# Kernel optimization log

Hardware: AMD Instinct MI355X
Metric: run time of the kernel (lower is better)

Reference implementation:

```python
import jax, jax.numpy as jnp
import numpy as np

N = 50000      # nodes
E = 800000     # edges (avg degree 16)
DIN = 128
HID = 128
OUT = 10       # classes
G = 64         # graphs in batch


def setup_inputs() -> dict:
    key = jax.random.key(0)
    ks = jax.random.split(key, 10)
    x = jax.random.normal(ks[0], (N, DIN), dtype=jnp.float32)
    edge_index = jax.random.randint(ks[1], (2, E), 0, N, dtype=jnp.int32)
    edge_weight = jax.random.uniform(ks[2], (E,), dtype=jnp.float32)
    batch = jnp.sort(jax.random.randint(ks[3], (N,), 0, G, dtype=jnp.int32))
    W1 = jax.random.normal(ks[4], (DIN, HID), dtype=jnp.float32) / np.sqrt(DIN)
    b1 = jnp.zeros((HID,), dtype=jnp.float32)
    W2 = jax.random.normal(ks[5], (HID, HID), dtype=jnp.float32) / np.sqrt(HID)
    b2 = jnp.zeros((HID,), dtype=jnp.float32)
    W3 = jax.random.normal(ks[6], (HID, OUT), dtype=jnp.float32) / np.sqrt(HID)
    b3 = jnp.zeros((OUT,), dtype=jnp.float32)
    return {"x": x, "edge_index": edge_index, "edge_weight": edge_weight,
            "batch": batch, "W1": W1, "b1": b1, "W2": W2, "b2": b2,
            "W3": W3, "b3": b3}


def _gcn_norm(edge_index, edge_weight, n_nodes):
    # PyG gcn_norm: add self-loops with weight 1, D^-1/2 (A+I) D^-1/2
    loop = jnp.arange(n_nodes, dtype=edge_index.dtype)
    src = jnp.concatenate([edge_index[0], loop])
    dst = jnp.concatenate([edge_index[1], loop])
    w = jnp.concatenate([edge_weight, jnp.ones((n_nodes,), edge_weight.dtype)])
    deg = jax.ops.segment_sum(w, dst, num_segments=n_nodes)
    dinv = jnp.where(deg > 0, jax.lax.rsqrt(deg), 0.0)
    norm = dinv[src] * w * dinv[dst]
    return src, dst, norm


def _gcn_conv(x, W, b, src, dst, norm, n_nodes):
    h = x @ W                                      # [N, F] dense transform
    msg = norm[:, None] * h[src]                   # gather + scale  [E+N, F]
    out = jax.ops.segment_sum(msg, dst, num_segments=n_nodes)  # scatter-add
    return out + b


def reference(x, edge_index, edge_weight, batch, W1, b1, W2, b2, W3, b3):
    src, dst, norm = _gcn_norm(edge_index, edge_weight, N)
    h = jax.nn.relu(_gcn_conv(x, W1, b1, src, dst, norm, N))
    h = jax.nn.relu(_gcn_conv(h, W2, b2, src, dst, norm, N))
    h = _gcn_conv(h, W3, b3, src, dst, norm, N)    # [N, OUT]
    # global_mean_pool over graph ids
    sums = jax.ops.segment_sum(h, batch, num_segments=G)          # [G, OUT]
    cnts = jax.ops.segment_sum(jnp.ones((N,), h.dtype), batch, num_segments=G)
    pooled = sums / jnp.maximum(cnts, 1.0)[:, None]
    return jax.nn.log_softmax(pooled, axis=1)
```

## Files before the change

### kernel.cpp

```cpp
#include <hip/hip_runtime.h>
#include <math.h>

#define NN 50000
#define EE 800000
#define GG 64
#define FD 128
#define OUTD 10
#define GB 782
#define BB 196
#define NBU 196
#define NBK 128
#define CH 6250
#define RCAP 8
#define TB 64

typedef __attribute__((ext_vector_type(8))) short s8v;
typedef __attribute__((ext_vector_type(4))) float f4v;

static __device__ inline unsigned short f2b(float f) {
    unsigned int u = __float_as_uint(f);
    return (unsigned short)((u + 0x7FFFu + ((u >> 16) & 1u)) >> 16);
}


__global__ __launch_bounds__(256) void k_histbounds(const float* __restrict__ W1,
        const float* __restrict__ W2, const float* __restrict__ W3,
        unsigned short* __restrict__ Wt1, unsigned short* __restrict__ Wt2,
        float* __restrict__ W3t, const int* __restrict__ dst, int* __restrict__ cnt2d,
        const int* __restrict__ batch, int* __restrict__ gstart) {
    int b = blockIdx.x;
    int tid = threadIdx.x;
    if (b < TB) {
        int i = b * 256 + tid;
        if (i < FD * FD) {
            int nn = i >> 7, k = i & 127;
            Wt1[i] = f2b(W1[k * FD + nn]);
            Wt2[i] = f2b(W2[k * FD + nn]);
        }
        if (i < FD * OUTD) {
            int col = i >> 7, row = i & 127;
            W3t[i] = W3[row * OUTD + col];
        }
    } else if (b < TB + NBK) {
        __shared__ unsigned hist[NBU];
        int blk = b - TB;
        if (tid < NBU) hist[tid] = 0;
        __syncthreads();
        int e0 = blk * CH;
        for (int e = e0 + tid; e < e0 + CH; e += 256)
            atomicAdd(&hist[(unsigned)dst[e] >> 8], 1u);
        __syncthreads();
        if (tid < NBU) cnt2d[tid * NBK + blk] = (int)hist[tid];
    } else {
        int i = (b - TB - NBK) * 256 + tid;
        if (i < NN) {
            int bb = batch[i];
            int bp = (i == 0) ? -1 : batch[i - 1];
            for (int g = bp + 1; g <= bb; ++g) gstart[g] = i;
            if (i == NN - 1)
                for (int g = bb + 1; g <= GG; ++g) gstart[g] = NN;
        }
    }
}


static __device__ inline void gemm_f32in_body(int bid, const float* __restrict__ A,
        const unsigned short* __restrict__ Wt, unsigned short* __restrict__ out, int n) {
    int tid = threadIdx.x;
    int wave = tid >> 6, lane = tid & 63;
    int quad = lane >> 4, c16 = lane & 15;
    int rowbase = bid * 64 + wave * 16;
    int rowA = rowbase + c16;
    if (rowA >= n) rowA = n - 1;
    f4v acc[8];
    #pragma unroll
    for (int t = 0; t < 8; ++t) acc[t] = (f4v){0.f, 0.f, 0.f, 0.f};
    #pragma unroll
    for (int k0 = 0; k0 < 128; k0 += 32) {
        const float* ap = A + (size_t)rowA * FD + k0 + quad * 8;
        float4 a0 = *(const float4*)ap;
        float4 a1 = *(const float4*)(ap + 4);
        s8v a;
        a[0] = (short)f2b(a0.x); a[1] = (short)f2b(a0.y);
        a[2] = (short)f2b(a0.z); a[3] = (short)f2b(a0.w);
        a[4] = (short)f2b(a1.x); a[5] = (short)f2b(a1.y);
        a[6] = (short)f2b(a1.z); a[7] = (short)f2b(a1.w);
        #pragma unroll
        for (int t = 0; t < 8; ++t) {
            s8v bb = *(const s8v*)(Wt + (size_t)(t * 16 + c16) * FD + k0 + quad * 8);
            acc[t] = __builtin_amdgcn_mfma_f32_16x16x32_bf16(a, bb, acc[t], 0, 0, 0);
        }
    }
    #pragma unroll
    for (int t = 0; t < 8; ++t) {
        #pragma unroll
        for (int r = 0; r < 4; ++r) {
            int row = rowbase + quad * 4 + r;
            if (row < n) out[(size_t)row * FD + t * 16 + c16] = f2b(acc[t][r]);
        }
    }
}

__global__ __launch_bounds__(256) void k_scatgemm(const int* __restrict__ src,
        const int* __restrict__ dst, const float* __restrict__ ew,
        const int* __restrict__ cnt2d, int* __restrict__ bbase_g, uint2* __restrict__ rec,
        const float* __restrict__ x, const unsigned short* __restrict__ Wt1,
        unsigned short* __restrict__ hA) {
    int b = blockIdx.x;
    int tid = threadIdx.x;
    if (b >= NBK) {
        gemm_f32in_body(b - NBK, x, Wt1, hA, NN);
        return;
    }
    __shared__ int colsum[NBU];
    __shared__ int ownoff[NBU];
    __shared__ unsigned cur[NBU];
    __shared__ int wtot_s[4];
    int blk = b;
    if (tid < NBU) {
        const int* c = cnt2d + tid * NBK;
        int own = 0, tot = 0;
        for (int k = 0; k < NBK; ++k) {
            int t = c[k];
            if (k < blk) own += t;
            tot += t;
        }
        ownoff[tid] = own;
        colsum[tid] = tot;
    }
    __syncthreads();
    {
        int lane = tid & 63, wv = tid >> 6;
        int v = (tid < NBU) ? colsum[tid] : 0;
        int s = v;
        #pragma unroll
        for (int off = 1; off < 64; off <<= 1) {
            int u = __shfl_up(s, off, 64);
            if (lane >= off) s += u;
        }
        if (lane == 63) wtot_s[wv] = s;
        __syncthreads();
        int pre = 0;
        for (int j = 0; j < wv; ++j) pre += wtot_s[j];
        int base = pre + s - v;
        if (tid < NBU) {
            cur[tid] = (unsigned)(base + ownoff[tid]);
            if (blk == 0) bbase_g[tid] = base;
        }
        if (blk == 0 && tid == NBU - 1) bbase_g[NBU] = base + v;
    }
    __syncthreads();
    int e0 = blk * CH;
    for (int e = e0 + tid; e < e0 + CH; e += 256) {
        int d = dst[e];
        unsigned bkt = (unsigned)d >> 8;
        unsigned pos = atomicAdd(&cur[bkt], 1u);
        rec[pos] = make_uint2(((unsigned)(d & 255) << 16) | (unsigned)src[e],
                              __float_as_uint(ew[e]));
    }
}


__global__ __launch_bounds__(1024) void k_rankfill(const uint2* __restrict__ rec,
        const int* __restrict__ bbase, int* __restrict__ rowptr, float* __restrict__ dinv_g,
        uint2* __restrict__ ent, unsigned short* __restrict__ rankb) {
    __shared__ unsigned cntS[256];
    __shared__ float wdegS[256];
    __shared__ int wtot_s[4];
    __shared__ int rowS[256];
    __shared__ float dinvS[256];
    int b = blockIdx.x;
    int tid = threadIdx.x;
    if (tid < 256) { cntS[tid] = 0; wdegS[tid] = 0.0f; }
    __syncthreads();
    int beg = bbase[b], end = bbase[b + 1];
    int s0 = beg + tid;
    uint2 rv[RCAP];
    unsigned rk[RCAP];
    #pragma unroll
    for (int k = 0; k < RCAP; ++k) {
        int s = s0 + k * 1024;
        if (s < end) {
            uint2 r = rec[s];
            unsigned dl = r.x >> 16;
            unsigned old = atomicAdd(&cntS[dl], 1u);
            atomicAdd(&wdegS[dl], __uint_as_float(r.y));
            rv[k] = r; rk[k] = old;
        }
    }
    for (int s = s0 + RCAP * 1024; s < end; s += 1024) {
        uint2 r = rec[s];
        unsigned dl = r.x >> 16;
        unsigned old = atomicAdd(&cntS[dl], 1u);
        atomicAdd(&wdegS[dl], __uint_as_float(r.y));
        rankb[s] = (unsigned short)old;
    }
    __syncthreads();
    {
        int lane = tid & 63, wv = tid >> 6;
        int v = (tid < 256) ? (int)cntS[tid] : 0;
        int s = v;
        #pragma unroll
        for (int off = 1; off < 64; off <<= 1) {
            int u = __shfl_up(s, off, 64);
            if (lane >= off) s += u;
        }
        if (tid < 256 && lane == 63) wtot_s[wv] = s;
        __syncthreads();
        if (tid < 256) {
            int pre = 0;
            for (int j = 0; j < wv; ++j) pre += wtot_s[j];
            int excl = pre + s - v;
            int node = b * 256 + tid;
            if (node < NN) {
                int r = beg + node + excl;
                rowS[tid] = r;
                rowptr[node] = r;
                float di = 1.0f / sqrtf(wdegS[tid] + 1.0f);
                dinvS[tid] = di;
                dinv_g[node] = di;
                ent[r + v] = make_uint2((unsigned)node, __float_as_uint(di));
            }
            if (node == NN - 1) rowptr[NN] = EE + NN;
        }
    }
    __syncthreads();
    #pragma unroll
    for (int k = 0; k < RCAP; ++k) {
        int s = s0 + k * 1024;
        if (s < end) {
            uint2 r = rv[k];
            unsigned dl = r.x >> 16;
            int pos = rowS[dl] + (int)rk[k];
            float val = __uint_as_float(r.y) * dinvS[dl];
            ent[pos] = make_uint2(r.x & 0xFFFFu, __float_as_uint(val));
        }
    }
    for (int s = s0 + RCAP * 1024; s < end; s += 1024) {
        uint2 r = rec[s];
        unsigned dl = r.x >> 16;
        int pos = rowS[dl] + (int)rankb[s];
        float val = __uint_as_float(r.y) * dinvS[dl];
        ent[pos] = make_uint2(r.x & 0xFFFFu, __float_as_uint(val));
    }
}


__global__ __launch_bounds__(256) void k_spmm_bf(const int* __restrict__ rowptr,
        const uint2* __restrict__ ent, const float* __restrict__ dinv,
        const unsigned short* __restrict__ tin, const float* __restrict__ bias,
        unsigned short* __restrict__ out, int n) {
    int w = (blockIdx.x * blockDim.x + threadIdx.x) >> 6;
    int lane = threadIdx.x & 63;
    if (w >= n) return;
    int c = lane & 15, g = lane >> 4;
    int beg = rowptr[w], end = rowptr[w + 1];
    float acc[8];
    #pragma unroll
    for (int j = 0; j < 8; ++j) acc[j] = 0.0f;
    int e0 = beg;
    for (; e0 + 16 <= end; e0 += 16) {
        uint2 en[4];
        float dv[4];
        uint4 t[4];
        #pragma unroll
        for (int u = 0; u < 4; ++u) en[u] = ent[e0 + 4 * u + g];
        #pragma unroll
        for (int u = 0; u < 4; ++u) dv[u] = dinv[en[u].x];
        #pragma unroll
        for (int u = 0; u < 4; ++u)
            t[u] = *(const uint4*)(tin + (size_t)en[u].x * FD + c * 8);
        #pragma unroll
        for (int u = 0; u < 4; ++u) {
            float v = __uint_as_float(en[u].y) * dv[u];
            acc[0] += v * __uint_as_float(t[u].x << 16);
            acc[1] += v * __uint_as_float(t[u].x & 0xFFFF0000u);
            acc[2] += v * __uint_as_float(t[u].y << 16);
            acc[3] += v * __uint_as_float(t[u].y & 0xFFFF0000u);
            acc[4] += v * __uint_as_float(t[u].z << 16);
            acc[5] += v * __uint_as_float(t[u].z & 0xFFFF0000u);
            acc[6] += v * __uint_as_float(t[u].w << 16);
            acc[7] += v * __uint_as_float(t[u].w & 0xFFFF0000u);
        }
    }
    for (; e0 < end; e0 += 4) {
        int e = e0 + g;
        uint2 en = (e < end) ? ent[e] : make_uint2(0u, 0u);
        float v = (e < end) ? __uint_as_float(en.y) * dinv[en.x] : 0.0f;
        uint4 t = *(const uint4*)(tin + (size_t)en.x * FD + c * 8);
        acc[0] += v * __uint_as_float(t.x << 16);
        acc[1] += v * __uint_as_float(t.x & 0xFFFF0000u);
        acc[2] += v * __uint_as_float(t.y << 16);
        acc[3] += v * __uint_as_float(t.y & 0xFFFF0000u);
        acc[4] += v * __uint_as_float(t.z << 16);
        acc[5] += v * __uint_as_float(t.z & 0xFFFF0000u);
        acc[6] += v * __uint_as_float(t.w << 16);
        acc[7] += v * __uint_as_float(t.w & 0xFFFF0000u);
    }
    #pragma unroll
    for (int j = 0; j < 8; ++j) {
        acc[j] += __shfl_xor(acc[j], 16, 64);
        acc[j] += __shfl_xor(acc[j], 32, 64);
    }
    if (g == 0) {
        float dself = dinv[w];
        uint4 r;
        float o[8];
        #pragma unroll
        for (int j = 0; j < 8; ++j)
            o[j] = fmaxf(acc[j] + bias[c * 8 + j], 0.0f) * dself;
        r.x = (unsigned)f2b(o[0]) | ((unsigned)f2b(o[1]) << 16);
        r.y = (unsigned)f2b(o[2]) | ((unsigned)f2b(o[3]) << 16);
        r.z = (unsigned)f2b(o[4]) | ((unsigned)f2b(o[5]) << 16);
        r.w = (unsigned)f2b(o[6]) | ((unsigned)f2b(o[7]) << 16);
        *(uint4*)(out + (size_t)w * FD + c * 8) = r;
    }
}


__global__ __launch_bounds__(256) void k_gemm_bf(const unsigned short* __restrict__ A,
        const unsigned short* __restrict__ Wt, unsigned short* __restrict__ out, int n) {
    int tid = threadIdx.x;
    int wave = tid >> 6, lane = tid & 63;
    int quad = lane >> 4, c16 = lane & 15;
    int rowbase = blockIdx.x * 64 + wave * 16;
    int rowA = rowbase + c16;
    if (rowA >= n) rowA = n - 1;
    f4v acc[8];
    #pragma unroll
    for (int t = 0; t < 8; ++t) acc[t] = (f4v){0.f, 0.f, 0.f, 0.f};
    #pragma unroll
    for (int k0 = 0; k0 < 128; k0 += 32) {
        s8v a = *(const s8v*)(A + (size_t)rowA * FD + k0 + quad * 8);
        #pragma unroll
        for (int t = 0; t < 8; ++t) {
            s8v b = *(const s8v*)(Wt + (size_t)(t * 16 + c16) * FD + k0 + quad * 8);
            acc[t] = __builtin_amdgcn_mfma_f32_16x16x32_bf16(a, b, acc[t], 0, 0, 0);
        }
    }
    #pragma unroll
    for (int t = 0; t < 8; ++t) {
        #pragma unroll
        for (int r = 0; r < 4; ++r) {
            int row = rowbase + quad * 4 + r;
            if (row < n) out[(size_t)row * FD + t * 16 + c16] = f2b(acc[t][r]);
        }
    }
}


__global__ __launch_bounds__(256) void k_spmm_w3(const int* __restrict__ rowptr,
        const uint2* __restrict__ ent, const float* __restrict__ dinv,
        const unsigned short* __restrict__ tin, const float* __restrict__ bias2,
        const float* __restrict__ W3t, float* __restrict__ outc, int n) {
    int tid = threadIdx.x;
    int w = (blockIdx.x * blockDim.x + tid) >> 6;
    int lane = tid & 63;
    if (w >= n) return;
    int c = lane & 15, g = lane >> 4;
    int beg = rowptr[w], end = rowptr[w + 1];
    float acc[8];
    #pragma unroll
    for (int j = 0; j < 8; ++j) acc[j] = 0.0f;
    int e0 = beg;
    for (; e0 + 16 <= end; e0 += 16) {
        uint2 en[4];
        uint4 t[4];
        #pragma unroll
        for (int u = 0; u < 4; ++u) en[u] = ent[e0 + 4 * u + g];
        #pragma unroll
        for (int u = 0; u < 4; ++u)
            t[u] = *(const uint4*)(tin + (size_t)en[u].x * FD + c * 8);
        #pragma unroll
        for (int u = 0; u < 4; ++u) {
            float v = __uint_as_float(en[u].y);
            acc[0] += v * __uint_as_float(t[u].x << 16);
            acc[1] += v * __uint_as_float(t[u].x & 0xFFFF0000u);
            acc[2] += v * __uint_as_float(t[u].y << 16);
            acc[3] += v * __uint_as_float(t[u].y & 0xFFFF0000u);
            acc[4] += v * __uint_as_float(t[u].z << 16);
            acc[5] += v * __uint_as_float(t[u].z & 0xFFFF0000u);
            acc[6] += v * __uint_as_float(t[u].w << 16);
            acc[7] += v * __uint_as_float(t[u].w & 0xFFFF0000u);
        }
    }
    for (; e0 < end; e0 += 4) {
        int e = e0 + g;
        uint2 en = (e < end) ? ent[e] : make_uint2(0u, 0u);
        float v = (e < end) ? __uint_as_float(en.y) : 0.0f;
        uint4 t = *(const uint4*)(tin + (size_t)en.x * FD + c * 8);
        acc[0] += v * __uint_as_float(t.x << 16);
        acc[1] += v * __uint_as_float(t.x & 0xFFFF0000u);
        acc[2] += v * __uint_as_float(t.y << 16);
        acc[3] += v * __uint_as_float(t.y & 0xFFFF0000u);
        acc[4] += v * __uint_as_float(t.z << 16);
        acc[5] += v * __uint_as_float(t.z & 0xFFFF0000u);
        acc[6] += v * __uint_as_float(t.w << 16);
        acc[7] += v * __uint_as_float(t.w & 0xFFFF0000u);
    }
    #pragma unroll
    for (int j = 0; j < 8; ++j) {
        acc[j] += __shfl_xor(acc[j], 16, 64);
        acc[j] += __shfl_xor(acc[j], 32, 64);
    }
    float b2r[8], o[8];
    *(float4*)&b2r[0] = *(const float4*)(bias2 + c * 8);
    *(float4*)&b2r[4] = *(const float4*)(bias2 + c * 8 + 4);
    #pragma unroll
    for (int j = 0; j < 8; ++j)
        o[j] = fmaxf(acc[j] + b2r[j], 0.0f);
    float w0[8], w1[8];
    *(float4*)&w0[0] = *(const float4*)(W3t + g * FD + c * 8);
    *(float4*)&w0[4] = *(const float4*)(W3t + g * FD + c * 8 + 4);
    *(float4*)&w1[0] = *(const float4*)(W3t + (g + 4) * FD + c * 8);
    *(float4*)&w1[4] = *(const float4*)(W3t + (g + 4) * FD + c * 8 + 4);
    float p0 = 0.0f, p1 = 0.0f, p2 = 0.0f;
    #pragma unroll
    for (int j = 0; j < 8; ++j) {
        p0 += o[j] * w0[j];
        p1 += o[j] * w1[j];
    }
    if (g < 2) {
        float w2[8];
        *(float4*)&w2[0] = *(const float4*)(W3t + (g + 8) * FD + c * 8);
        *(float4*)&w2[4] = *(const float4*)(W3t + (g + 8) * FD + c * 8 + 4);
        #pragma unroll
        for (int j = 0; j < 8; ++j) p2 += o[j] * w2[j];
    }
    #pragma unroll
    for (int off = 1; off < 16; off <<= 1) {
        p0 += __shfl_xor(p0, off, 64);
        p1 += __shfl_xor(p1, off, 64);
        p2 += __shfl_xor(p2, off, 64);
    }
    if (c == 0) {
        float dself = dinv[w];
        float* op = outc + (size_t)w * OUTD;
        op[g] = p0 * dself;
        op[g + 4] = p1 * dself;
        if (g < 2) op[g + 8] = p2 * dself;
    }
}


__global__ void k_spmm10(const int* __restrict__ rowptr, const uint2* __restrict__ ent,
        const float* __restrict__ tin, const float* __restrict__ bias,
        float* __restrict__ out, int n) {
    int t = blockIdx.x * blockDim.x + threadIdx.x;
    int node = t / OUTD;
    int c = t - node * OUTD;
    if (node >= n) return;
    int beg = rowptr[node], end = rowptr[node + 1];
    float acc = 0.0f;
    for (int e = beg; e < end; ++e) {
        uint2 en = ent[e];
        acc += __uint_as_float(en.y) * tin[(size_t)en.x * OUTD + c];
    }
    out[(size_t)node * OUTD + c] = acc + bias[c];
}


__global__ __launch_bounds__(256) void k_poolfin(const float* __restrict__ h,
        const int* __restrict__ gstart, float* __restrict__ out) {
    int g = blockIdx.x;
    int beg = gstart[g], end = gstart[g + 1];
    int tid = threadIdx.x;
    int lane = tid & 63, wv = tid >> 6;
    float acc[OUTD];
    #pragma unroll
    for (int c = 0; c < OUTD; ++c) acc[c] = 0.0f;
    for (int i = beg + tid; i < end; i += 256) {
        const float* hp = h + (size_t)i * OUTD;
        #pragma unroll
        for (int c = 0; c < OUTD; ++c) acc[c] += hp[c];
    }
    #pragma unroll
    for (int off = 32; off >= 1; off >>= 1)
        #pragma unroll
        for (int c = 0; c < OUTD; ++c) acc[c] += __shfl_down(acc[c], off, 64);
    __shared__ float ws[4][OUTD];
    if (lane == 0)
        #pragma unroll
        for (int c = 0; c < OUTD; ++c) ws[wv][c] = acc[c];
    __syncthreads();
    if (tid == 0) {
        float cf = fmaxf((float)(end - beg), 1.0f);
        float v[OUTD], m = -1e30f;
        #pragma unroll
        for (int c = 0; c < OUTD; ++c) {
            v[c] = (ws[0][c] + ws[1][c] + ws[2][c] + ws[3][c]) / cf;
            m = fmaxf(m, v[c]);
        }
        float s = 0.0f;
        #pragma unroll
        for (int c = 0; c < OUTD; ++c) s += expf(v[c] - m);
        float l = logf(s);
        #pragma unroll
        for (int c = 0; c < OUTD; ++c) out[g * OUTD + c] = v[c] - m - l;
    }
}


extern "C" void kernel_launch(void* const* d_in, const int* in_sizes, int n_in,
                              void* d_out, int out_size, void* d_ws, size_t ws_size,
                              hipStream_t stream) {
    const float* x   = (const float*)d_in[0];
    const int*   ei  = (const int*)d_in[1];
    const float* ew  = (const float*)d_in[2];
    const int*   bat = (const int*)d_in[3];
    const float* W1  = (const float*)d_in[4];
    const float* b1  = (const float*)d_in[5];
    const float* W2  = (const float*)d_in[6];
    const float* b2  = (const float*)d_in[7];
    const float* W3  = (const float*)d_in[8];
    const float* b3  = (const float*)d_in[9];
    float* out = (float*)d_out;

    const int* src = ei;
    const int* dst = ei + EE;

    char* p = (char*)d_ws;
    auto alloc = [&](size_t bytes) -> void* {
        void* r = (void*)p;
        p += (bytes + 255) & ~(size_t)255;
        return r;
    };
    int*            cnt2d  = (int*)  alloc((size_t)NBU * NBK * 4);
    int*            bbase  = (int*)  alloc((size_t)(NBU + 1) * 4);
    uint2*          rec    = (uint2*)alloc((size_t)EE * 8);
    unsigned short* rankb  = (unsigned short*)alloc((size_t)EE * 2);
    float*          dinv   = (float*)alloc((size_t)NN * 4);
    int*            rowptr = (int*)  alloc((size_t)(NN + 1) * 4);
    uint2*          ent    = (uint2*)alloc((size_t)(EE + NN) * 8);
    unsigned short* Wt1    = (unsigned short*)alloc((size_t)FD * FD * 2);
    unsigned short* Wt2    = (unsigned short*)alloc((size_t)FD * FD * 2);
    float*          W3t    = (float*)alloc((size_t)FD * OUTD * 4);
    unsigned short* hA     = (unsigned short*)alloc((size_t)NN * FD * 2);
    unsigned short* hB     = (unsigned short*)alloc((size_t)NN * FD * 2);
    float*          bufC   = (float*)alloc((size_t)NN * OUTD * 4);
    float*          bufD   = (float*)alloc((size_t)NN * OUTD * 4);
    int*            gstart = (int*)  alloc((size_t)(GG + 1) * 4);
    (void)ws_size; (void)in_sizes; (void)n_in; (void)out_size;

    const int B = 256;
    k_histbounds<<<TB + NBK + BB, B, 0, stream>>>(W1, W2, W3, Wt1, Wt2, W3t,
                                                  dst, cnt2d, bat, gstart);
    k_scatgemm<<<NBK + GB, B, 0, stream>>>(src, dst, ew, cnt2d, bbase, rec, x, Wt1, hA);
    k_rankfill<<<NBU, 1024, 0, stream>>>(rec, bbase, rowptr, dinv, ent, rankb);
    k_spmm_bf <<<(NN * 64 + B - 1) / B, B, 0, stream>>>(rowptr, ent, dinv, hA, b1, hB, NN);
    k_gemm_bf <<<GB, B, 0, stream>>>(hB, Wt2, hA, NN);
    k_spmm_w3 <<<(NN * 64 + B - 1) / B, B, 0, stream>>>(rowptr, ent, dinv, hA, b2, W3t, bufC, NN);
    k_spmm10  <<<(NN * OUTD + B - 1) / B, B, 0, stream>>>(rowptr, ent, bufC, b3, bufD, NN);
    k_poolfin <<<GG, 256, 0, stream>>>(bufD, gstart, out);
}
```

Measured before the change: 254.8 us.

## Split edge binning into more chunks and precompute bucket offsets in a separate scan kernel

```diff
diff --git a/kernel.cpp b/kernel.cpp
--- a/kernel.cpp
+++ b/kernel.cpp
@@ -9,8 +9,8 @@
 #define GB 782
 #define BB 196
 #define NBU 196
-#define NBK 128
-#define CH 6250
+#define NBK 512
+#define CH 1563
 #define RCAP 8
 #define TB 64
 
@@ -27,7 +27,7 @@
         const float* __restrict__ W2, const float* __restrict__ W3,
         unsigned short* __restrict__ Wt1, unsigned short* __restrict__ Wt2,
         float* __restrict__ W3t, const int* __restrict__ dst, int* __restrict__ cnt2d,
-        const int* __restrict__ batch, int* __restrict__ gstart) {
+        const int* __restrict__ batch, int* __restrict__ gstart, int* __restrict__ bflag) {
     int b = blockIdx.x;
     int tid = threadIdx.x;
     if (b < TB) {
@@ -41,13 +41,15 @@
             int col = i >> 7, row = i & 127;
             W3t[i] = W3[row * OUTD + col];
         }
+        if (i < NBU) bflag[i] = 0;
     } else if (b < TB + NBK) {
         __shared__ unsigned hist[NBU];
         int blk = b - TB;
         if (tid < NBU) hist[tid] = 0;
         __syncthreads();
         int e0 = blk * CH;
-        for (int e = e0 + tid; e < e0 + CH; e += 256)
+        int eend = e0 + CH < EE ? e0 + CH : EE;
+        for (int e = e0 + tid; e < eend; e += 256)
             atomicAdd(&hist[(unsigned)dst[e] >> 8], 1u);
         __syncthreads();
         if (tid < NBU) cnt2d[tid * NBK + blk] = (int)hist[tid];
@@ -64,6 +66,53 @@
 }
 
 
+__global__ __launch_bounds__(512) void k_off2d(const int* __restrict__ cnt2d,
+        int* __restrict__ off2d, int* __restrict__ bbase, int* __restrict__ bsum,
+        int* __restrict__ bflag) {
+    __shared__ int wtot[8];
+    __shared__ int base_sh;
+    int b = blockIdx.x;
+    int tid = threadIdx.x;
+    int lane = tid & 63, wv = tid >> 6;
+    int v = cnt2d[b * NBK + tid];
+    int s = v;
+    #pragma unroll
+    for (int off = 1; off < 64; off <<= 1) {
+        int u = __shfl_up(s, off, 64);
+        if (lane >= off) s += u;
+    }
+    if (lane == 63) wtot[wv] = s;
+    __syncthreads();
+    int wpre = 0, tot = 0;
+    #pragma unroll
+    for (int j = 0; j < 8; ++j) {
+        if (j < wv) wpre += wtot[j];
+        tot += wtot[j];
+    }
+    int excl = wpre + s - v;
+    if (tid == 0) {
+        bsum[b] = tot;
+        __hip_atomic_store(&bflag[b], 1, __ATOMIC_RELEASE, __HIP_MEMORY_SCOPE_AGENT);
+    }
+    if (tid < 64) {
+        int acc = 0;
+        for (int q = tid; q < b; q += 64) {
+            while (__hip_atomic_load(&bflag[q], __ATOMIC_ACQUIRE,
+                                     __HIP_MEMORY_SCOPE_AGENT) == 0) {}
+            acc += bsum[q];
+        }
+        #pragma unroll
+        for (int off = 32; off >= 1; off >>= 1) acc += __shfl_xor(acc, off, 64);
+        if (tid == 0) base_sh = acc;
+    }
+    __syncthreads();
+    int base = base_sh;
+    off2d[tid * NBU + b] = base + excl;
+    if (tid == 0) bbase[b] = base;
+    if (b == NBU - 1 && tid == 0) bbase[NBU] = base + tot;
+}
+
+
 static __device__ inline void gemm_f32in_body(int bid, const float* __restrict__ A,
         const unsigned short* __restrict__ Wt, unsigned short* __restrict__ out, int n) {
     int tid = threadIdx.x;
@@ -103,7 +152,7 @@
 
 __global__ __launch_bounds__(256) void k_scatgemm(const int* __restrict__ src,
         const int* __restrict__ dst, const float* __restrict__ ew,
-        const int* __restrict__ cnt2d, int* __restrict__ bbase_g, uint2* __restrict__ rec,
+        const int* __restrict__ off2d, uint2* __restrict__ rec,
         const float* __restrict__ x, const unsigned short* __restrict__ Wt1,
         unsigned short* __restrict__ hA) {
     int b = blockIdx.x;
@@ -112,46 +161,12 @@
         gemm_f32in_body(b - NBK, x, Wt1, hA, NN);
         return;
     }
-    __shared__ int colsum[NBU];
-    __shared__ int ownoff[NBU];
     __shared__ unsigned cur[NBU];
-    __shared__ int wtot_s[4];
-    int blk = b;
-    if (tid < NBU) {
-        const int* c = cnt2d + tid * NBK;
-        int own = 0, tot = 0;
-        for (int k = 0; k < NBK; ++k) {
-            int t = c[k];
-            if (k < blk) own += t;
-            tot += t;
-        }
-        ownoff[tid] = own;
-        colsum[tid] = tot;
-    }
-    __syncthreads();
-    {
-        int lane = tid & 63, wv = tid >> 6;
-        int v = (tid < NBU) ? colsum[tid] : 0;
-        int s = v;
-        #pragma unroll
-        for (int off = 1; off < 64; off <<= 1) {
-            int u = __shfl_up(s, off, 64);
-            if (lane >= off) s += u;
-        }
-        if (lane == 63) wtot_s[wv] = s;
-        __syncthreads();
-        int pre = 0;
-        for (int j = 0; j < wv; ++j) pre += wtot_s[j];
-        int base = pre + s - v;
-        if (tid < NBU) {
-            cur[tid] = (unsigned)(base + ownoff[tid]);
-            if (blk == 0) bbase_g[tid] = base;
-        }
-        if (blk == 0 && tid == NBU - 1) bbase_g[NBU] = base + v;
-    }
-    __syncthreads();
-    int e0 = blk * CH;
-    for (int e = e0 + tid; e < e0 + CH; e += 256) {
+    if (tid < NBU) cur[tid] = (unsigned)off2d[b * NBU + tid];
+    __syncthreads();
+    int e0 = b * CH;
+    int eend = e0 + CH < EE ? e0 + CH : EE;
+    for (int e = e0 + tid; e < eend; e += 256) {
         int d = dst[e];
         unsigned bkt = (unsigned)d >> 8;
         unsigned pos = atomicAdd(&cur[bkt], 1u);
@@ -526,7 +541,10 @@
         return r;
     };
     int*            cnt2d  = (int*)  alloc((size_t)NBU * NBK * 4);
+    int*            off2d  = (int*)  alloc((size_t)NBK * NBU * 4);
     int*            bbase  = (int*)  alloc((size_t)(NBU + 1) * 4);
+    int*            bsum   = (int*)  alloc((size_t)NBU * 4);
+    int*            bflag  = (int*)  alloc((size_t)NBU * 4);
     uint2*          rec    = (uint2*)alloc((size_t)EE * 8);
     unsigned short* rankb  = (unsigned short*)alloc((size_t)EE * 2);
     float*          dinv   = (float*)alloc((size_t)NN * 4);
@@ -544,8 +562,9 @@
 
     const int B = 256;
     k_histbounds<<<TB + NBK + BB, B, 0, stream>>>(W1, W2, W3, Wt1, Wt2, W3t,
-                                                  dst, cnt2d, bat, gstart);
-    k_scatgemm<<<NBK + GB, B, 0, stream>>>(src, dst, ew, cnt2d, bbase, rec, x, Wt1, hA);
+                                                  dst, cnt2d, bat, gstart, bflag);
+    k_off2d   <<<NBU, 512, 0, stream>>>(cnt2d, off2d, bbase, bsum, bflag);
+    k_scatgemm<<<NBK + GB, B, 0, stream>>>(src, dst, ew, off2d, rec, x, Wt1, hA);
     k_rankfill<<<NBU, 1024, 0, stream>>>(rec, bbase, rowptr, dinv, ent, rankb);
     k_spmm_bf <<<(NN * 64 + B - 1) / B, B, 0, stream>>>(rowptr, ent, dinv, hA, b1, hB, NN);
     k_gemm_bf <<<GB, B, 0, stream>>>(hB, Wt2, hA, NN);
```

Result: no change. 257.6 us (+1.1%).
